# Optimization experiments

Hardware: AMD Instinct MI355X
Metric: run time of the kernel (lower is better)

## Reference

```python
import jax, jax.numpy as jnp
import numpy as np

NH = 16  # n_heads

def setup_inputs() -> dict:
    key = jax.random.key(0)
    ks = jax.random.split(key, 5)
    B, T, D = 2, 2048, 2048
    scale = 0.02
    return {
        "x": jax.random.normal(ks[0], (B, T, D), dtype=jnp.float32),
        "Wq": jax.random.normal(ks[1], (D, D), dtype=jnp.float32) * scale,
        "Wk": jax.random.normal(ks[2], (D, D), dtype=jnp.float32) * scale,
        "Wv": jax.random.normal(ks[3], (D, D), dtype=jnp.float32) * scale,
        "Wo": jax.random.normal(ks[4], (D, D), dtype=jnp.float32) * scale,
    }

def reference(x, Wq, Wk, Wv, Wo):
    B, T, D = x.shape
    hd = D // NH
    # torch nn.Linear(d,d,bias=False): y = x @ W.T
    q = (x @ Wq.T).reshape(B, T, NH, hd).transpose(0, 2, 1, 3)  # [B,H,T,hd]
    k = (x @ Wk.T).reshape(B, T, NH, hd).transpose(0, 2, 1, 3)
    v = (x @ Wv.T).reshape(B, T, NH, hd).transpose(0, 2, 1, 3)
    att = jnp.einsum('bhtd,bhsd->bhts', q, k) / jnp.sqrt(jnp.asarray(hd, x.dtype))
    neg = jnp.finfo(att.dtype).min
    mask = jnp.triu(jnp.full((T, T), neg, dtype=att.dtype), k=1)  # causal
    att = att + mask
    w = jax.nn.softmax(att, axis=-1)
    z = jnp.einsum('bhts,bhsd->bhtd', w, v)  # [B,H,T,hd]
    z = z.transpose(0, 2, 1, 3).reshape(B, T, D)
    return z @ Wo.T
```

## Files before the change

### kernel.cpp

```cpp
#include <hip/hip_runtime.h>
#include <hip/hip_bf16.h>
#include <math.h>


typedef __attribute__((ext_vector_type(4))) float  f32x4;
typedef __attribute__((ext_vector_type(8))) __bf16 bf16x8;

union Pack8 { __bf16 h[8]; uint4 u; };
union Pack4 { __bf16 h[4]; uint2 u; };

__device__ __forceinline__ void async16(const void* g, void* l) {
    __builtin_amdgcn_global_load_lds((const __attribute__((address_space(1))) void*)g,
                                     (__attribute__((address_space(3))) void*)l, 16, 0, 0);
}

struct CvtArgs { const float* s[5]; __bf16* d[5]; };

__global__ __launch_bounds__(256) void cvt_all(CvtArgs a) {
    int i = blockIdx.x * 256 + threadIdx.x;
    int t, off;
    if (i < (1 << 20)) { t = 0; off = i; }
    else { int j = i - (1 << 20); t = 1 + (j >> 19); off = j & ((1 << 19) - 1); }
    const float4* s = (const float4*)a.s[t] + (size_t)off * 2;
    float4 f0 = s[0], f1 = s[1];
    Pack8 pk;
    pk.h[0] = (__bf16)f0.x; pk.h[1] = (__bf16)f0.y;
    pk.h[2] = (__bf16)f0.z; pk.h[3] = (__bf16)f0.w;
    pk.h[4] = (__bf16)f1.x; pk.h[5] = (__bf16)f1.y;
    pk.h[6] = (__bf16)f1.z; pk.h[7] = (__bf16)f1.w;
    ((uint4*)a.d[t])[off] = pk.u;
}

__global__ __launch_bounds__(512, 2) void gemm_qkv(const __bf16* __restrict__ A,
        const __bf16* __restrict__ Wq, const __bf16* __restrict__ Wk,
        const __bf16* __restrict__ Wv,
        __bf16* __restrict__ Qo, __bf16* __restrict__ Ko, __bf16* __restrict__ Vt) {
    constexpr int K = 2048, N = 2048, MT = 4096, NT = K / 64;
    __shared__ __bf16 lds[2][32768];
    const int tid  = threadIdx.x;
    const int w    = tid >> 6;
    const int lane = tid & 63;
    const int lm   = lane & 15;
    const int quad = lane >> 4;
    const int wm   = w >> 2;
    const int wn   = w & 3;

    const int bid   = blockIdx.x;
    const int seg   = bid >> 7;
    const int mt    = (bid >> 3) & 15;
    const int nt    = bid & 7;
    const int mrow0 = mt * 256;
    const int ncol0 = nt * 256;
    const __bf16* B = (seg == 0) ? Wq : (seg == 1) ? Wk : Wv;

    const int fmA0 = ((w >= 4) ? 8 : 0) + (w & 3);
    const int fnB0 = ((w >> 1) << 2) | (w & 1);
    const __bf16* gA0 = A + (size_t)(mrow0 + fmA0 * 16 + lm) * K + quad * 8;
    const __bf16* gA1 = gA0 + (size_t)64 * K;
    const __bf16* gB0 = B + (size_t)(ncol0 + fnB0 * 16 + lm) * K + quad * 8;
    const __bf16* gB1 = gB0 + (size_t)32 * K;

    f32x4  acc[8][4] = {};
    bf16x8 ra0[4][2], ra1[4][2], rb0[2][2], rb1[2][2];

#define STAGE_A0(t_, bufp_) do {                                            \
        async16(gA0 + (size_t)(t_) * 64,      (bufp_) + fmA0 * 1024);       \
        async16(gA0 + (size_t)(t_) * 64 + 32, (bufp_) + fmA0 * 1024 + 512); \
    } while (0)
#define STAGE_A1(t_, bufp_) do {                                                  \
        async16(gA1 + (size_t)(t_) * 64,      (bufp_) + (fmA0 + 4) * 1024);       \
        async16(gA1 + (size_t)(t_) * 64 + 32, (bufp_) + (fmA0 + 4) * 1024 + 512); \
    } while (0)
#define STAGE_B0(t_, bufp_) do {                                                    \
        async16(gB0 + (size_t)(t_) * 64,      (bufp_) + 16384 + fnB0 * 1024);       \
        async16(gB0 + (size_t)(t_) * 64 + 32, (bufp_) + 16384 + fnB0 * 1024 + 512); \
    } while (0)
#define STAGE_B1(t_, bufp_) do {                                                          \
        async16(gB1 + (size_t)(t_) * 64,      (bufp_) + 16384 + (fnB0 + 2) * 1024);       \
        async16(gB1 + (size_t)(t_) * 64 + 32, (bufp_) + 16384 + (fnB0 + 2) * 1024 + 512); \
    } while (0)

#define READ_A(dst, bufp_, mh) do {                                              \
        const __bf16* ap_ = (bufp_) + wm * 8192 + (mh) * 4096;                   \
        _Pragma("unroll") for (int i_ = 0; i_ < 4; ++i_)                         \
        _Pragma("unroll") for (int kf_ = 0; kf_ < 2; ++kf_)                      \
            dst[i_][kf_] = *(const bf16x8*)(ap_ + i_ * 1024 + kf_ * 512 + lane * 8); \
    } while (0)
#define READ_B(dst, bufp_, nh) do {                                              \
        const __bf16* bp_ = (bufp_) + 16384 + wn * 4096 + (nh) * 2048;           \
        _Pragma("unroll") for (int j_ = 0; j_ < 2; ++j_)                         \
        _Pragma("unroll") for (int kf_ = 0; kf_ < 2; ++kf_)                      \
            dst[j_][kf_] = *(const bf16x8*)(bp_ + j_ * 1024 + kf_ * 512 + lane * 8); \
    } while (0)
#define MMA(mh, nh, Ar, Br) do {                                                 \
        __builtin_amdgcn_s_setprio(1);                                           \
        _Pragma("unroll") for (int kf_ = 0; kf_ < 2; ++kf_)                      \
        _Pragma("unroll") for (int i_ = 0; i_ < 4; ++i_)                         \
        _Pragma("unroll") for (int j_ = 0; j_ < 2; ++j_)                         \
            acc[(mh) * 4 + i_][(nh) * 2 + j_] =                                  \
                __builtin_amdgcn_mfma_f32_16x16x32_bf16(                         \
                    Ar[i_][kf_], Br[j_][kf_],                                    \
                    acc[(mh) * 4 + i_][(nh) * 2 + j_], 0, 0, 0);                 \
        __builtin_amdgcn_s_setprio(0);                                           \
    } while (0)

    {
        __bf16* b0p = &lds[0][0];
        __bf16* b1p = &lds[0][0] + 32768;
        STAGE_B0(0, b0p); STAGE_A0(0, b0p); STAGE_A1(0, b0p); STAGE_B1(0, b0p);
        STAGE_B0(1, b1p); STAGE_A0(1, b1p); STAGE_A1(1, b1p); STAGE_B1(1, b1p);
        asm volatile("s_waitcnt vmcnt(8)" ::: "memory");
        __builtin_amdgcn_s_barrier();
    }

    for (int t = 0; t < NT; ++t) {
        __bf16* bufp = &lds[0][0] + (size_t)(t & 1) * 32768;
        const bool st = (t + 2 < NT);
        READ_A(ra0, bufp, 0);
        READ_B(rb0, bufp, 0);
        __builtin_amdgcn_s_barrier();
        MMA(0, 0, ra0, rb0);
        __builtin_amdgcn_s_barrier();
        READ_A(ra1, bufp, 1);
        if (st) { STAGE_B0(t + 2, bufp); STAGE_A0(t + 2, bufp); }
        __builtin_amdgcn_s_barrier();
        MMA(1, 0, ra1, rb0);
        __builtin_amdgcn_s_barrier();
        READ_B(rb1, bufp, 1);
        if (st) STAGE_A1(t + 2, bufp);
        __builtin_amdgcn_s_barrier();
        MMA(0, 1, ra0, rb1);
        __builtin_amdgcn_s_barrier();
        if (st) {
            asm volatile("s_waitcnt vmcnt(6)" ::: "memory");
            STAGE_B1(t + 2, bufp);
        } else {
            asm volatile("s_waitcnt vmcnt(0)" ::: "memory");
        }
        __builtin_amdgcn_s_barrier();
        MMA(1, 1, ra1, rb1);
        __builtin_amdgcn_s_barrier();
    }
#undef STAGE_A0
#undef STAGE_A1
#undef STAGE_B0
#undef STAGE_B1
#undef READ_A
#undef READ_B
#undef MMA

    const int wrow = mrow0 + wm * 128;
    const int wcol = ncol0 + wn * 64;
    if (seg < 2) {
        __bf16* C = seg ? Ko : Qo;
#pragma unroll
        for (int mi = 0; mi < 8; ++mi)
#pragma unroll
            for (int nj = 0; nj < 4; ++nj)
#pragma unroll
                for (int r = 0; r < 4; ++r)
                    C[(size_t)(wrow + mi * 16 + quad * 4 + r) * N +
                      wcol + nj * 16 + lm] = (__bf16)acc[mi][nj][r];
    } else {
#pragma unroll
        for (int mi = 0; mi < 8; ++mi)
#pragma unroll
            for (int nj = 0; nj < 4; ++nj) {
                Pack4 p;
#pragma unroll
                for (int r = 0; r < 4; ++r) p.h[r] = (__bf16)acc[mi][nj][r];
                *(uint2*)&Vt[(size_t)(wcol + nj * 16 + lm) * MT +
                             wrow + mi * 16 + quad * 4] = p.u;
            }
    }
}

__global__ __launch_bounds__(512, 2) void gemm_wo(const __bf16* __restrict__ A,
                                                  const __bf16* __restrict__ B,
                                                  float* __restrict__ C) {
    constexpr int K = 2048, N = 2048, NT = K / 64;
    __shared__ __bf16 lds[2][24576];
    const int tid  = threadIdx.x;
    const int w    = tid >> 6;
    const int lane = tid & 63;
    const int lm   = lane & 15;
    const int quad = lane >> 4;
    const int wm   = w >> 2;
    const int wn   = w & 3;

    const int bid   = blockIdx.x;
    const int mt    = bid >> 3;
    const int nt    = bid & 7;
    const int mrow0 = mt * 128;
    const int ncol0 = nt * 256;

    const __bf16* gA  = A + (size_t)(mrow0 + w * 16 + lm) * K + quad * 8;
    const __bf16* gB0 = B + (size_t)(ncol0 + w * 16 + lm) * K + quad * 8;
    const __bf16* gB1 = gB0 + (size_t)128 * K;

    f32x4  acc[4][4] = {};
    bf16x8 ra[4][2], rb0[2][2], rb1[2][2];

#define WSTAGE_A(t_, bufp_) do {                                            \
        async16(gA + (size_t)(t_) * 64,      (bufp_) + (w * 2) * 512);      \
        async16(gA + (size_t)(t_) * 64 + 32, (bufp_) + (w * 2 + 1) * 512);  \
    } while (0)
#define WSTAGE_B(t_, bufp_) do {                                                       \
        async16(gB0 + (size_t)(t_) * 64,      (bufp_) + 8192 + (w * 2) * 512);         \
        async16(gB0 + (size_t)(t_) * 64 + 32, (bufp_) + 8192 + (w * 2 + 1) * 512);     \
        async16(gB1 + (size_t)(t_) * 64,      (bufp_) + 8192 + ((8 + w) * 2) * 512);   \
        async16(gB1 + (size_t)(t_) * 64 + 32, (bufp_) + 8192 + ((8 + w) * 2 + 1) * 512); \
    } while (0)

#define WREAD_A(bufp_) do {                                                      \
        _Pragma("unroll") for (int i_ = 0; i_ < 4; ++i_)                         \
        _Pragma("unroll") for (int kf_ = 0; kf_ < 2; ++kf_)                      \
            ra[i_][kf_] = *(const bf16x8*)((bufp_) +                             \
                ((wm * 4 + i_) * 2 + kf_) * 512 + lane * 8);                     \
    } while (0)
#define WREAD_B(dst, bufp_, half) do {                                           \
        _Pragma("unroll") for (int j_ = 0; j_ < 2; ++j_)                         \
        _Pragma("unroll") for (int kf_ = 0; kf_ < 2; ++kf_)                      \
            dst[j_][kf_] = *(const bf16x8*)((bufp_) + 8192 +                     \
                ((wn * 4 + (half) * 2 + j_) * 2 + kf_) * 512 + lane * 8);        \
    } while (0)
#define WMMA(nh, rb) do {                                                        \
        __builtin_amdgcn_s_setprio(1);                                           \
        _Pragma("unroll") for (int kf_ = 0; kf_ < 2; ++kf_)                      \
        _Pragma("unroll") for (int i_ = 0; i_ < 4; ++i_)                         \
        _Pragma("unroll") for (int j_ = 0; j_ < 2; ++j_)                         \
            acc[i_][(nh) * 2 + j_] = __builtin_amdgcn_mfma_f32_16x16x32_bf16(    \
                ra[i_][kf_], rb[j_][kf_], acc[i_][(nh) * 2 + j_], 0, 0, 0);      \
        __builtin_amdgcn_s_setprio(0);                                           \
    } while (0)

    WSTAGE_A(0, &lds[0][0]);
    WSTAGE_B(0, &lds[0][0]);
    WSTAGE_A(1, &lds[1][0]);
    asm volatile("s_waitcnt vmcnt(2)" ::: "memory");
    __builtin_amdgcn_s_barrier();

    for (int t = 0; t < NT; ++t) {
        __bf16* bufp = &lds[0][0] + (size_t)(t & 1) * 24576;
        __bf16* bufo = &lds[0][0] + (size_t)((t + 1) & 1) * 24576;
        WREAD_A(bufp);
        WREAD_B(rb0, bufp, 0);
        if (t + 1 < NT) WSTAGE_B(t + 1, bufo);
        __builtin_amdgcn_s_barrier();
        WMMA(0, rb0);
        __builtin_amdgcn_s_barrier();
        WREAD_B(rb1, bufp, 1);
        if (t + 2 < NT) {
            WSTAGE_A(t + 2, bufp);
            asm volatile("s_waitcnt vmcnt(2)" ::: "memory");
        } else {
            asm volatile("s_waitcnt vmcnt(0)" ::: "memory");
        }
        __builtin_amdgcn_s_barrier();
        WMMA(1, rb1);
        __builtin_amdgcn_s_barrier();
    }
#undef WSTAGE_A
#undef WSTAGE_B
#undef WREAD_A
#undef WREAD_B
#undef WMMA

    const int wrow = mrow0 + wm * 64;
    const int wcol = ncol0 + wn * 64;
#pragma unroll
    for (int mi = 0; mi < 4; ++mi)
#pragma unroll
        for (int nj = 0; nj < 4; ++nj)
#pragma unroll
            for (int r = 0; r < 4; ++r)
                C[(size_t)(wrow + mi * 16 + quad * 4 + r) * N +
                  wcol + nj * 16 + lm] = acc[mi][nj][r];
}

__global__ __launch_bounds__(256) void attn6(const __bf16* __restrict__ Q,
                                             const __bf16* __restrict__ K,
                                             const __bf16* __restrict__ Vt,
                                             __bf16* __restrict__ Z) {
    constexpr int T = 2048, D = 2048, MT = 4096, PS = 72;
    __shared__ __bf16 KVf[2][32 * 512];
    __shared__ __bf16 Pf[4 * 16 * PS];
    const int tid  = threadIdx.x;
    const int w    = tid >> 6;
    const int lane = tid & 63;
    const int lm   = lane & 15;
    const int quad = lane >> 4;
    const int f    = blockIdx.x;
    const int bh   = ((f >> 7) << 3) | (f & 7);
    const int pair = (f >> 3) & 15;
    const int b    = bh >> 4;
    const int h    = bh & 15;

    const size_t qkbase = (size_t)b * T * D + (size_t)h * 128;
    const __bf16* Qh = Q + qkbase;
    const __bf16* Kh = K + qkbase;
    const __bf16* Vh = Vt + (size_t)(h * 128) * MT + (size_t)b * T;
    __bf16* Zh = Z + qkbase;

    bf16x8 ones;
#pragma unroll
    for (int i = 0; i < 8; ++i) ones[i] = (__bf16)1.0f;

    const float c = 0.08838834764831845f;
    __bf16* pw = Pf + w * (16 * PS);

#define ATTN_ISSUE(kv0, buf)                                                     \
    do {                                                                         \
        _Pragma("unroll")                                                        \
        for (int i = 0; i < 4; ++i) {                                            \
            const int fk = w * 4 + i;                                            \
            const int nt = fk >> 2, kk = fk & 3;                                 \
            async16(Kh + (size_t)((kv0) + nt * 16 + lm) * D + kk * 32 + quad * 8,\
                    KVf[buf] + fk * 512);                                        \
            const int on = fk >> 1, kc = fk & 1;                                 \
            async16(Vh + (size_t)(on * 16 + lm) * MT + (kv0) + kc * 32 + quad * 8,\
                    KVf[buf] + (16 + fk) * 512);                                 \
        }                                                                        \
    } while (0)

    for (int ph = 0; ph < 2; ++ph) {
        const int j  = ph ? 31 - pair : pair;
        const int q0 = j * 64 + w * 16;

        bf16x8 qf[4];
#pragma unroll
        for (int kk = 0; kk < 4; ++kk)
            qf[kk] = *(const bf16x8*)(Qh + (size_t)(q0 + lm) * D + kk * 32 + quad * 8);

        f32x4 o[8] = {};
        f32x4 osum = {};

        __syncthreads();
        ATTN_ISSUE(0, 0);
        int buf = 0;

        for (int t = 0; t <= j; ++t) {
            __syncthreads();
            if (t < j) ATTN_ISSUE((t + 1) * 64, buf ^ 1);
            const __bf16* Kc = KVf[buf];
            const __bf16* Vc = KVf[buf] + 16 * 512;
            buf ^= 1;
            const int kv0 = t * 64;

            f32x4 s[4] = {};
#pragma unroll
            for (int nt = 0; nt < 4; ++nt)
#pragma unroll
                for (int kk = 0; kk < 4; ++kk) {
                    bf16x8 kfr = *(const bf16x8*)(Kc + (nt * 4 + kk) * 512 + lane * 8);
                    s[nt] = __builtin_amdgcn_mfma_f32_16x16x32_bf16(qf[kk], kfr, s[nt], 0, 0, 0);
                }

            const bool diag = (t == j);
#pragma unroll
            for (int nt = 0; nt < 4; ++nt)
#pragma unroll
                for (int r = 0; r < 4; ++r) {
                    float v = s[nt][r];
                    if (diag && (kv0 + nt * 16 + lm > q0 + quad * 4 + r)) v = -1e30f;
                    s[nt][r] = __expf(fmaf(v, c, -4.0f));
                }

#pragma unroll
            for (int nt = 0; nt < 4; ++nt)
#pragma unroll
                for (int r = 0; r < 4; ++r)
                    pw[(quad * 4 + r) * PS + nt * 16 + lm] = (__bf16)s[nt][r];

            bf16x8 pf[2];
#pragma unroll
            for (int kc = 0; kc < 2; ++kc)
                pf[kc] = *(const bf16x8*)(pw + lm * PS + kc * 32 + quad * 8);

#pragma unroll
            for (int kc = 0; kc < 2; ++kc) {
                osum = __builtin_amdgcn_mfma_f32_16x16x32_bf16(pf[kc], ones, osum, 0, 0, 0);
#pragma unroll
                for (int on = 0; on < 8; ++on) {
                    bf16x8 vf = *(const bf16x8*)(Vc + (on * 2 + kc) * 512 + lane * 8);
                    o[on] = __builtin_amdgcn_mfma_f32_16x16x32_bf16(pf[kc], vf, o[on], 0, 0, 0);
                }
            }
        }

        float inv[4];
#pragma unroll
        for (int r = 0; r < 4; ++r) inv[r] = 1.f / osum[r];
#pragma unroll
        for (int on = 0; on < 8; ++on)
#pragma unroll
            for (int r = 0; r < 4; ++r)
                Zh[(size_t)(q0 + quad * 4 + r) * D + on * 16 + lm] =
                    (__bf16)(o[on][r] * inv[r]);
    }
#undef ATTN_ISSUE
}

extern "C" void kernel_launch(void* const* d_in, const int* in_sizes, int n_in,
                              void* d_out, int out_size, void* d_ws, size_t ws_size,
                              hipStream_t stream) {
    const float* x  = (const float*)d_in[0];
    const float* Wq = (const float*)d_in[1];
    const float* Wk = (const float*)d_in[2];
    const float* Wv = (const float*)d_in[3];
    const float* Wo = (const float*)d_in[4];
    const int D = 2048, M = 4096;
    const size_t SZ_X = (size_t)M * D;
    const size_t SZ_W = (size_t)D * D;

    __bf16* xb  = (__bf16*)d_ws;
    __bf16* Wqb = xb + SZ_X;
    __bf16* Wkb = Wqb + SZ_W;
    __bf16* Wvb = Wkb + SZ_W;
    __bf16* Wob = Wvb + SZ_W;
    __bf16* Qb  = Wob + SZ_W;
    __bf16* Kb  = Qb + SZ_X;
    __bf16* Vtb = Kb + SZ_X;
    __bf16* Zb  = xb;

    CvtArgs ca;
    ca.s[0] = x;  ca.s[1] = Wq;  ca.s[2] = Wk;  ca.s[3] = Wv;  ca.s[4] = Wo;
    ca.d[0] = xb; ca.d[1] = Wqb; ca.d[2] = Wkb; ca.d[3] = Wvb; ca.d[4] = Wob;
    cvt_all<<<12288, 256, 0, stream>>>(ca);

    gemm_qkv<<<384, 512, 0, stream>>>(xb, Wqb, Wkb, Wvb, Qb, Kb, Vtb);

    attn6<<<512, 256, 0, stream>>>(Qb, Kb, Vtb, Zb);

    gemm_wo<<<256, 512, 0, stream>>>(Zb, Wob, (float*)d_out);
}
```

Before: 401.6 us.

## Fuse Q/K/V projections per block sharing the A tile across three weights

Each QKV GEMM block now computes all three projections for a 128x256 output tile, loading the activation tile once and reusing it for Wq, Wk and Wv, with a 32-wide K step. The grid shrinks from 384 to 256 blocks, which removes the partial second wave and cuts redundant A loads. In exchange, each thread holds more accumulators, and the finer K step adds more barrier iterations.

Result: faster. 382.1 us (-4.8%).

```diff
diff --git a/kernel.cpp b/kernel.cpp
--- a/kernel.cpp
+++ b/kernel.cpp
@@ -35,8 +35,9 @@
         const __bf16* __restrict__ Wq, const __bf16* __restrict__ Wk,
         const __bf16* __restrict__ Wv,
         __bf16* __restrict__ Qo, __bf16* __restrict__ Ko, __bf16* __restrict__ Vt) {
-    constexpr int K = 2048, N = 2048, MT = 4096, NT = K / 64;
-    __shared__ __bf16 lds[2][32768];
+    constexpr int K = 2048, N = 2048, MT = 4096, NT = K / 32;
+    constexpr int BUF = 28672;
+    __shared__ __bf16 lds[2 * BUF];
     const int tid  = threadIdx.x;
     const int w    = tid >> 6;
     const int lane = tid & 63;
@@ -46,133 +47,104 @@
     const int wn   = w & 3;
 
     const int bid   = blockIdx.x;
-    const int seg   = bid >> 7;
-    const int mt    = (bid >> 3) & 15;
+    const int mt    = bid >> 3;
     const int nt    = bid & 7;
-    const int mrow0 = mt * 256;
+    const int mrow0 = mt * 128;
     const int ncol0 = nt * 256;
-    const __bf16* B = (seg == 0) ? Wq : (seg == 1) ? Wk : Wv;
-
-    const int fmA0 = ((w >= 4) ? 8 : 0) + (w & 3);
-    const int fnB0 = ((w >> 1) << 2) | (w & 1);
-    const __bf16* gA0 = A + (size_t)(mrow0 + fmA0 * 16 + lm) * K + quad * 8;
-    const __bf16* gA1 = gA0 + (size_t)64 * K;
-    const __bf16* gB0 = B + (size_t)(ncol0 + fnB0 * 16 + lm) * K + quad * 8;
-    const __bf16* gB1 = gB0 + (size_t)32 * K;
-
-    f32x4  acc[8][4] = {};
-    bf16x8 ra0[4][2], ra1[4][2], rb0[2][2], rb1[2][2];
-
-#define STAGE_A0(t_, bufp_) do {                                            \
-        async16(gA0 + (size_t)(t_) * 64,      (bufp_) + fmA0 * 1024);       \
-        async16(gA0 + (size_t)(t_) * 64 + 32, (bufp_) + fmA0 * 1024 + 512); \
-    } while (0)
-#define STAGE_A1(t_, bufp_) do {                                                  \
-        async16(gA1 + (size_t)(t_) * 64,      (bufp_) + (fmA0 + 4) * 1024);       \
-        async16(gA1 + (size_t)(t_) * 64 + 32, (bufp_) + (fmA0 + 4) * 1024 + 512); \
-    } while (0)
-#define STAGE_B0(t_, bufp_) do {                                                    \
-        async16(gB0 + (size_t)(t_) * 64,      (bufp_) + 16384 + fnB0 * 1024);       \
-        async16(gB0 + (size_t)(t_) * 64 + 32, (bufp_) + 16384 + fnB0 * 1024 + 512); \
-    } while (0)
-#define STAGE_B1(t_, bufp_) do {                                                          \
-        async16(gB1 + (size_t)(t_) * 64,      (bufp_) + 16384 + (fnB0 + 2) * 1024);       \
-        async16(gB1 + (size_t)(t_) * 64 + 32, (bufp_) + 16384 + (fnB0 + 2) * 1024 + 512); \
-    } while (0)
-
-#define READ_A(dst, bufp_, mh) do {                                              \
-        const __bf16* ap_ = (bufp_) + wm * 8192 + (mh) * 4096;                   \
-        _Pragma("unroll") for (int i_ = 0; i_ < 4; ++i_)                         \
-        _Pragma("unroll") for (int kf_ = 0; kf_ < 2; ++kf_)                      \
-            dst[i_][kf_] = *(const bf16x8*)(ap_ + i_ * 1024 + kf_ * 512 + lane * 8); \
-    } while (0)
-#define READ_B(dst, bufp_, nh) do {                                              \
-        const __bf16* bp_ = (bufp_) + 16384 + wn * 4096 + (nh) * 2048;           \
-        _Pragma("unroll") for (int j_ = 0; j_ < 2; ++j_)                         \
-        _Pragma("unroll") for (int kf_ = 0; kf_ < 2; ++kf_)                      \
-            dst[j_][kf_] = *(const bf16x8*)(bp_ + j_ * 1024 + kf_ * 512 + lane * 8); \
-    } while (0)
-#define MMA(mh, nh, Ar, Br) do {                                                 \
-        __builtin_amdgcn_s_setprio(1);                                           \
-        _Pragma("unroll") for (int kf_ = 0; kf_ < 2; ++kf_)                      \
-        _Pragma("unroll") for (int i_ = 0; i_ < 4; ++i_)                         \
-        _Pragma("unroll") for (int j_ = 0; j_ < 2; ++j_)                         \
-            acc[(mh) * 4 + i_][(nh) * 2 + j_] =                                  \
-                __builtin_amdgcn_mfma_f32_16x16x32_bf16(                         \
-                    Ar[i_][kf_], Br[j_][kf_],                                    \
-                    acc[(mh) * 4 + i_][(nh) * 2 + j_], 0, 0, 0);                 \
-        __builtin_amdgcn_s_setprio(0);                                           \
+
+    const __bf16* gA  = A  + (size_t)(mrow0 + w * 16 + lm) * K + quad * 8;
+    const size_t  bofs = (size_t)(ncol0 + (2 * w) * 16 + lm) * K + quad * 8;
+    const __bf16* gB0 = Wq + bofs;
+    const __bf16* gB1 = Wk + bofs;
+    const __bf16* gB2 = Wv + bofs;
+
+    f32x4  acc[3][4][4] = {};
+    bf16x8 ra[4], rb[4];
+
+#define STAGE_A(t_, bufp_) \
+        async16(gA + (size_t)(t_) * 32, (bufp_) + w * 512)
+#define STAGE_B(s_, glo_, t_, bufp_) do {                                          \
+        async16((glo_) + (size_t)(t_) * 32,                                        \
+                (bufp_) + 4096 + (s_) * 8192 + (2 * w) * 512);                     \
+        async16((glo_) + (size_t)16 * K + (size_t)(t_) * 32,                       \
+                (bufp_) + 4096 + (s_) * 8192 + (2 * w + 1) * 512);                 \
+    } while (0)
+
+#define READ_A(bufp_) do {                                                         \
+        _Pragma("unroll") for (int i_ = 0; i_ < 4; ++i_)                           \
+            ra[i_] = *(const bf16x8*)((bufp_) + (wm * 4 + i_) * 512 + lane * 8);   \
+    } while (0)
+#define READ_B(s_, bufp_) do {                                                     \
+        _Pragma("unroll") for (int j_ = 0; j_ < 4; ++j_)                           \
+            rb[j_] = *(const bf16x8*)((bufp_) + 4096 + (s_) * 8192 +               \
+                                      (wn * 4 + j_) * 512 + lane * 8);             \
+    } while (0)
+#define MMA_S(s_) do {                                                             \
+        __builtin_amdgcn_s_setprio(1);                                             \
+        _Pragma("unroll") for (int i_ = 0; i_ < 4; ++i_)                           \
+        _Pragma("unroll") for (int j_ = 0; j_ < 4; ++j_)                           \
+            acc[s_][i_][j_] = __builtin_amdgcn_mfma_f32_16x16x32_bf16(             \
+                ra[i_], rb[j_], acc[s_][i_][j_], 0, 0, 0);                         \
+        __builtin_amdgcn_s_setprio(0);                                             \
     } while (0)
 
     {
-        __bf16* b0p = &lds[0][0];
-        __bf16* b1p = &lds[0][0] + 32768;
-        STAGE_B0(0, b0p); STAGE_A0(0, b0p); STAGE_A1(0, b0p); STAGE_B1(0, b0p);
-        STAGE_B0(1, b1p); STAGE_A0(1, b1p); STAGE_A1(1, b1p); STAGE_B1(1, b1p);
-        asm volatile("s_waitcnt vmcnt(8)" ::: "memory");
+        __bf16* b0 = &lds[0];
+        __bf16* b1 = &lds[0] + BUF;
+        STAGE_A(0, b0); STAGE_B(0, gB0, 0, b0); STAGE_B(1, gB1, 0, b0); STAGE_B(2, gB2, 0, b0);
+        STAGE_A(1, b1); STAGE_B(0, gB0, 1, b1); STAGE_B(1, gB1, 1, b1); STAGE_B(2, gB2, 1, b1);
+        asm volatile("s_waitcnt vmcnt(7)" ::: "memory");
         __builtin_amdgcn_s_barrier();
     }
 
     for (int t = 0; t < NT; ++t) {
-        __bf16* bufp = &lds[0][0] + (size_t)(t & 1) * 32768;
+        __bf16* bufp = &lds[0] + (size_t)(t & 1) * BUF;
         const bool st = (t + 2 < NT);
-        READ_A(ra0, bufp, 0);
-        READ_B(rb0, bufp, 0);
-        __builtin_amdgcn_s_barrier();
-        MMA(0, 0, ra0, rb0);
-        __builtin_amdgcn_s_barrier();
-        READ_A(ra1, bufp, 1);
-        if (st) { STAGE_B0(t + 2, bufp); STAGE_A0(t + 2, bufp); }
-        __builtin_amdgcn_s_barrier();
-        MMA(1, 0, ra1, rb0);
-        __builtin_amdgcn_s_barrier();
-        READ_B(rb1, bufp, 1);
-        if (st) STAGE_A1(t + 2, bufp);
-        __builtin_amdgcn_s_barrier();
-        MMA(0, 1, ra0, rb1);
+        READ_A(bufp);
+        READ_B(0, bufp);
+        __builtin_amdgcn_s_barrier();
+        if (st) { STAGE_A(t + 2, bufp); STAGE_B(0, gB0, t + 2, bufp); }
+        MMA_S(0);
+        READ_B(1, bufp);
+        __builtin_amdgcn_s_barrier();
+        if (st) STAGE_B(1, gB1, t + 2, bufp);
+        MMA_S(1);
+        READ_B(2, bufp);
         __builtin_amdgcn_s_barrier();
         if (st) {
-            asm volatile("s_waitcnt vmcnt(6)" ::: "memory");
-            STAGE_B1(t + 2, bufp);
+            STAGE_B(2, gB2, t + 2, bufp);
+            asm volatile("s_waitcnt vmcnt(7)" ::: "memory");
         } else {
             asm volatile("s_waitcnt vmcnt(0)" ::: "memory");
         }
-        __builtin_amdgcn_s_barrier();
-        MMA(1, 1, ra1, rb1);
+        MMA_S(2);
         __builtin_amdgcn_s_barrier();
     }
-#undef STAGE_A0
-#undef STAGE_A1
-#undef STAGE_B0
-#undef STAGE_B1
+#undef STAGE_A
+#undef STAGE_B
 #undef READ_A
 #undef READ_B
-#undef MMA
-
-    const int wrow = mrow0 + wm * 128;
+#undef MMA_S
+
+    const int wrow = mrow0 + wm * 64;
     const int wcol = ncol0 + wn * 64;
-    if (seg < 2) {
-        __bf16* C = seg ? Ko : Qo;
-#pragma unroll
-        for (int mi = 0; mi < 8; ++mi)
-#pragma unroll
-            for (int nj = 0; nj < 4; ++nj)
-#pragma unroll
-                for (int r = 0; r < 4; ++r)
-                    C[(size_t)(wrow + mi * 16 + quad * 4 + r) * N +
-                      wcol + nj * 16 + lm] = (__bf16)acc[mi][nj][r];
-    } else {
-#pragma unroll
-        for (int mi = 0; mi < 8; ++mi)
-#pragma unroll
-            for (int nj = 0; nj < 4; ++nj) {
-                Pack4 p;
-#pragma unroll
-                for (int r = 0; r < 4; ++r) p.h[r] = (__bf16)acc[mi][nj][r];
-                *(uint2*)&Vt[(size_t)(wcol + nj * 16 + lm) * MT +
-                             wrow + mi * 16 + quad * 4] = p.u;
+#pragma unroll
+    for (int mi = 0; mi < 4; ++mi)
+#pragma unroll
+        for (int nj = 0; nj < 4; ++nj) {
+#pragma unroll
+            for (int r = 0; r < 4; ++r) {
+                Qo[(size_t)(wrow + mi * 16 + quad * 4 + r) * N +
+                   wcol + nj * 16 + lm] = (__bf16)acc[0][mi][nj][r];
+                Ko[(size_t)(wrow + mi * 16 + quad * 4 + r) * N +
+                   wcol + nj * 16 + lm] = (__bf16)acc[1][mi][nj][r];
             }
-    }
+            Pack4 p;
+#pragma unroll
+            for (int r = 0; r < 4; ++r) p.h[r] = (__bf16)acc[2][mi][nj][r];
+            *(uint2*)&Vt[(size_t)(wcol + nj * 16 + lm) * MT +
+                         wrow + mi * 16 + quad * 4] = p.u;
+        }
 }
 
 __global__ __launch_bounds__(512, 2) void gemm_wo(const __bf16* __restrict__ A,
@@ -428,7 +400,7 @@
     ca.d[0] = xb; ca.d[1] = Wqb; ca.d[2] = Wkb; ca.d[3] = Wvb; ca.d[4] = Wob;
     cvt_all<<<12288, 256, 0, stream>>>(ca);
 
-    gemm_qkv<<<384, 512, 0, stream>>>(xb, Wqb, Wkb, Wvb, Qb, Kb, Vtb);
+    gemm_qkv<<<256, 512, 0, stream>>>(xb, Wqb, Wkb, Wvb, Qb, Kb, Vtb);
 
     attn6<<<512, 256, 0, stream>>>(Qb, Kb, Vtb, Zb);
 
```
